# Optimization experiments

Hardware: AMD Instinct MI355X
Metric: run time of the kernel (lower is better)

## Reference

```python
import jax, jax.numpy as jnp
import numpy as np

MODEL_D = 512
N_HEADS = 8
D_K = 64
D_V = 64
EPS = 1e-5


def _layer_norm(x, g, b):
    mu = jnp.mean(x, axis=-1, keepdims=True)
    var = jnp.mean((x - mu) ** 2, axis=-1, keepdims=True)
    return (x - mu) * jax.lax.rsqrt(var + EPS) * g + b


def setup_inputs() -> dict:
    key = jax.random.key(0)
    ks = jax.random.split(key, 8)
    B, S = 8, 1024
    smiles = jax.random.normal(ks[0], (B, S, MODEL_D), dtype=jnp.float32)
    # causal mask: True where attention is disallowed (masked_fill semantics)
    mask = jnp.broadcast_to(jnp.triu(jnp.ones((S, S), dtype=bool), k=1), (B, S, S))
    sd = 1.0 / np.sqrt(MODEL_D)
    w_q = jax.random.normal(ks[1], (MODEL_D, N_HEADS * D_K), dtype=jnp.float32) * sd
    w_k = jax.random.normal(ks[2], (MODEL_D, N_HEADS * D_K), dtype=jnp.float32) * sd
    w_v = jax.random.normal(ks[3], (MODEL_D, N_HEADS * D_V), dtype=jnp.float32) * sd
    w_o = jax.random.normal(ks[4], (N_HEADS * D_V, MODEL_D), dtype=jnp.float32) * sd
    w1 = jax.random.normal(ks[5], (MODEL_D, 4 * MODEL_D), dtype=jnp.float32) * sd
    w2 = jax.random.normal(ks[6], (4 * MODEL_D, MODEL_D), dtype=jnp.float32) * (1.0 / np.sqrt(4 * MODEL_D))
    ln1_g = jnp.ones((MODEL_D,), jnp.float32)
    ln1_b = jnp.zeros((MODEL_D,), jnp.float32)
    ln2_g = jnp.ones((MODEL_D,), jnp.float32)
    ln2_b = jnp.zeros((MODEL_D,), jnp.float32)
    return {"smiles": smiles, "mask": mask, "w_q": w_q, "w_k": w_k, "w_v": w_v,
            "w_o": w_o, "ln1_g": ln1_g, "ln1_b": ln1_b, "w1": w1, "w2": w2,
            "ln2_g": ln2_g, "ln2_b": ln2_b}


def reference(smiles, mask, w_q, w_k, w_v, w_o, ln1_g, ln1_b, w1, w2, ln2_g, ln2_b):
    B, S, _ = smiles.shape
    # QKV projections -> [B, H, S, d]
    q = (smiles @ w_q).reshape(B, S, N_HEADS, D_K).transpose(0, 2, 1, 3)
    k = (smiles @ w_k).reshape(B, S, N_HEADS, D_K).transpose(0, 2, 1, 3)
    v = (smiles @ w_v).reshape(B, S, N_HEADS, D_V).transpose(0, 2, 1, 3)
    scores = jnp.einsum("bhqd,bhkd->bhqk", q, k) / np.sqrt(D_K)
    scores = jnp.where(mask[:, None, :, :], jnp.float32(-1e9), scores)
    attention = jax.nn.softmax(scores, axis=-1)
    ctx = jnp.einsum("bhqk,bhkd->bhqd", attention, v)
    ctx = ctx.transpose(0, 2, 1, 3).reshape(B, S, N_HEADS * D_V)
    attn_out = _layer_norm(ctx @ w_o + smiles, ln1_g, ln1_b)
    ffn = jax.nn.relu(attn_out @ w1) @ w2
    out = _layer_norm(ffn + attn_out, ln2_g, ln2_b)
    return out, attention
```

## Files before the change

kernel.cpp:

```cpp
#include <hip/hip_runtime.h>
#include <math.h>

#define BATCH 8
#define SEQ   1024
#define DMODEL 512
#define NHEADS 8
#define DKV   64
#define DFF   2048
#define ROWS  (BATCH * SEQ)
#define QKLD  1536

typedef __attribute__((ext_vector_type(8))) short short8;
typedef __attribute__((ext_vector_type(4))) float f32x4;

__device__ __forceinline__ short f2bf(float f) {
    unsigned u = __float_as_uint(f);
    u += 0x7FFFu + ((u >> 16) & 1u);
    return (short)(u >> 16);
}
__device__ __forceinline__ float bf2f(short s) {
    return __uint_as_float(((unsigned)(unsigned short)s) << 16);
}

#define GLD16(g, l) __builtin_amdgcn_global_load_lds( \
    (const __attribute__((address_space(1))) void*)(g), \
    (__attribute__((address_space(3))) void*)(l), 16, 0, 0)

__device__ __forceinline__ void stage128x32(const short* __restrict__ g, int ld,
                                            short* lds, int tid) {
    const int w = tid >> 6;
#pragma unroll
    for (int i = 0; i < 2; ++i) {
        const int L = i * 256 + tid;
        const int r = L >> 2, c = (L & 3) << 3;
        GLD16(g + (size_t)r * ld + c, lds + (size_t)(i * 256 + (w << 6)) * 8);
    }
}

template<int OUT_BF16, int RELU>
__global__ __launch_bounds__(256) void gemm_bt(const short* __restrict__ A,
                                               const short* __restrict__ Bt,
                                               void* __restrict__ Cv,
                                               int K, int lda, int ldb, int ldc,
                                               int qcols) {
    __shared__ short As[2][128 * 32];
    __shared__ short Bs[2][128 * 32];
    const int tid = threadIdx.x;

    const int nx = gridDim.x;
    const int nwg = nx * gridDim.y;
    const int flat = blockIdx.y * nx + blockIdx.x;
    const int swz = (flat & 7) * (nwg >> 3) + (flat >> 3);
    const int m0 = (swz / nx) * 128, n0 = (swz % nx) * 128;

    const int w = tid >> 6, lane = tid & 63;
    const int wr = (w >> 1) * 64, wc = (w & 1) * 64;
    const int lrow = lane & 15, hi = lane >> 4;

    f32x4 acc[4][4];
#pragma unroll
    for (int m = 0; m < 4; ++m)
#pragma unroll
        for (int n = 0; n < 4; ++n) acc[m][n] = {0.f, 0.f, 0.f, 0.f};

    const short* Ab = A + (size_t)m0 * lda;
    const short* Bb = Bt + (size_t)n0 * ldb;
    const int nt = K >> 5;

    stage128x32(Ab, lda, As[0], tid);
    stage128x32(Bb, ldb, Bs[0], tid);
    __syncthreads();

    int cur = 0;
    for (int t = 0; t < nt; ++t) {
        if (t + 1 < nt) {
            stage128x32(Ab + (size_t)(t + 1) * 32, lda, As[cur ^ 1], tid);
            stage128x32(Bb + (size_t)(t + 1) * 32, ldb, Bs[cur ^ 1], tid);
        }

        short8 af[4], bfr[4];
#pragma unroll
        for (int m = 0; m < 4; ++m)
            af[m] = *(const short8*)&As[cur][(size_t)(wr + m * 16 + lrow) * 32 + hi * 8];
#pragma unroll
        for (int n = 0; n < 4; ++n)
            bfr[n] = *(const short8*)&Bs[cur][(size_t)(wc + n * 16 + lrow) * 32 + hi * 8];
#pragma unroll
        for (int m = 0; m < 4; ++m)
#pragma unroll
            for (int n = 0; n < 4; ++n)
                acc[m][n] = __builtin_amdgcn_mfma_f32_16x16x32_bf16(bfr[n], af[m], acc[m][n], 0, 0, 0);

        __syncthreads();
        cur ^= 1;
    }

    const int orow = m0 + wr + lrow;
    const int ocol0 = n0 + wc + hi * 4;
#pragma unroll
    for (int m = 0; m < 4; ++m)
#pragma unroll
        for (int n = 0; n < 4; ++n) {
            const int col = ocol0 + n * 16;
            const float cs = (col < qcols) ? 0.125f : 1.0f;
            float v0 = acc[m][n][0], v1 = acc[m][n][1], v2 = acc[m][n][2], v3 = acc[m][n][3];
            if (RELU) {
                v0 = fmaxf(v0, 0.f); v1 = fmaxf(v1, 0.f);
                v2 = fmaxf(v2, 0.f); v3 = fmaxf(v3, 0.f);
            }
            v0 *= cs; v1 *= cs; v2 *= cs; v3 *= cs;
            const size_t off = (size_t)(orow + m * 16) * ldc + col;
            if (OUT_BF16) {
                short4 st = { f2bf(v0), f2bf(v1), f2bf(v2), f2bf(v3) };
                *(short4*)((short*)Cv + off) = st;
            } else {
                float4 st = { v0, v1, v2, v3 };
                *(float4*)((float*)Cv + off) = st;
            }
        }
}

__global__ __launch_bounds__(256, 2) void fused_attn(const short* __restrict__ Q,
                                                     const short* __restrict__ K,
                                                     const short* __restrict__ Vt,
                                                     float* __restrict__ attnP,
                                                     short* __restrict__ ctx) {
    const int flat = blockIdx.y * 8 + blockIdx.x;
    const int swz  = (flat & 7) * 64 + (flat >> 3);
    const int bh = swz >> 3, it = 7 - (swz & 7);
    const int b = bh >> 3, h = bh & 7;

    __shared__ short Qs[128 * 64];
    __shared__ short KVs[2][128 * 64];
    __shared__ short Ps[128 * 128];
    float* rsum = (float*)Ps;

    const int tid = threadIdx.x;
    const int w = tid >> 6, lane = tid & 63;
    const int wr = (w >> 1) * 64, wc2 = (w & 1);
    const int lrow = lane & 15, hi = lane >> 4;
    const size_t base = (size_t)b * SEQ * QKLD + h * DKV;
    float* aprow = attnP + (size_t)bh * SEQ * SEQ;

    auto stage_k = [&](int kt, short* dst) {
#pragma unroll
        for (int i = 0; i < 4; ++i) {
            const int L = i * 256 + tid;
            const int r = L >> 3, sc = ((L & 7) ^ (r & 7)) * 8;
            GLD16(K + base + (size_t)(kt * 128 + r) * QKLD + sc,
                  dst + (size_t)(i * 256 + (w << 6)) * 8);
        }
    };
    auto stage_v = [&](int kt, short* dst) {
#pragma unroll
        for (int i = 0; i < 4; ++i) {
            const int L = i * 256 + tid;
            const int r = L >> 4, sc = ((L & 15) ^ (r & 7)) * 8;
            GLD16(Vt + (size_t)(bh * DKV + r) * SEQ + kt * 128 + sc,
                  dst + (size_t)(i * 256 + (w << 6)) * 8);
        }
    };
    auto qkt = [&](const short* Ks, f32x4 s[4][4]) {
#pragma unroll
        for (int m = 0; m < 4; ++m)
#pragma unroll
            for (int n = 0; n < 4; ++n) s[m][n] = {0.f, 0.f, 0.f, 0.f};
#pragma unroll
        for (int sk = 0; sk < 2; ++sk) {
            short8 qf[4], kf[4];
#pragma unroll
            for (int m = 0; m < 4; ++m) {
                const int r = wr + m * 16 + lrow;
                qf[m] = *(const short8*)((const char*)Qs + r * 128 + ((hi * 16 + sk * 64) ^ ((r & 7) << 4)));
            }
#pragma unroll
            for (int n = 0; n < 4; ++n) {
                const int r = wc2 * 64 + n * 16 + lrow;
                kf[n] = *(const short8*)((const char*)Ks + r * 128 + ((hi * 16 + sk * 64) ^ ((r & 7) << 4)));
            }
#pragma unroll
            for (int m = 0; m < 4; ++m)
#pragma unroll
                for (int n = 0; n < 4; ++n)
                    s[m][n] = __builtin_amdgcn_mfma_f32_16x16x32_bf16(kf[n], qf[m], s[m][n], 0, 0, 0);
        }
    };

    {
        const int nz4 = (7 - it) * 32;
        if (nz4 > 0) {
            for (int r = tid >> 5; r < 128; r += 8) {
                float4* rp = (float4*)(aprow + (size_t)(it * 128 + r) * SEQ + (it + 1) * 128);
                for (int c = tid & 31; c < nz4; c += 32)
                    rp[c] = make_float4(0.f, 0.f, 0.f, 0.f);
            }
        }
    }

#pragma unroll
    for (int i = 0; i < 4; ++i) {
        const int L = i * 256 + tid;
        const int r = L >> 3, sc = ((L & 7) ^ (r & 7)) * 8;
        GLD16(Q + base + (size_t)(it * 128 + r) * QKLD + sc,
              Qs + (size_t)(i * 256 + (w << 6)) * 8);
    }
    stage_k(0, KVs[0]);
    stage_v(0, KVs[1]);
    __syncthreads();

    float rs[4] = {0.f, 0.f, 0.f, 0.f};
    f32x4 o[4][2];
#pragma unroll
    for (int m = 0; m < 4; ++m)
#pragma unroll
        for (int n = 0; n < 2; ++n) o[m][n] = {0.f, 0.f, 0.f, 0.f};

    for (int kt = 0; kt <= it; ++kt) {
        f32x4 s[4][4];
        qkt(KVs[0], s);

        const bool diag = (kt == it);
#pragma unroll
        for (int m = 0; m < 4; ++m) {
            const int q = wr + m * 16 + lrow;
#pragma unroll
            for (int n = 0; n < 4; ++n) {
                const int k0 = wc2 * 64 + n * 16 + hi * 4;
                float p0 = __expf(s[m][n][0]);
                float p1 = __expf(s[m][n][1]);
                float p2 = __expf(s[m][n][2]);
                float p3 = __expf(s[m][n][3]);
                if (diag) {
                    if (k0 + 0 > q) p0 = 0.f;
                    if (k0 + 1 > q) p1 = 0.f;
                    if (k0 + 2 > q) p2 = 0.f;
                    if (k0 + 3 > q) p3 = 0.f;
                }
                rs[m] += (p0 + p1) + (p2 + p3);
                short4 ph = { f2bf(p0), f2bf(p1), f2bf(p2), f2bf(p3) };
                *(short4*)((char*)Ps + q * 256 + ((k0 * 2) ^ ((q & 7) << 4))) = ph;
            }
        }
        __syncthreads();
        if (kt < it) stage_k(kt + 1, KVs[0]);

#pragma unroll
        for (int sk = 0; sk < 4; ++sk) {
            short8 pf[4], vf[2];
#pragma unroll
            for (int m = 0; m < 4; ++m) {
                const int r = wr + m * 16 + lrow;
                pf[m] = *(const short8*)((const char*)Ps + r * 256 + ((hi * 16 + sk * 64) ^ ((r & 7) << 4)));
            }
#pragma unroll
            for (int n = 0; n < 2; ++n) {
                const int r = wc2 * 32 + n * 16 + lrow;
                vf[n] = *(const short8*)((const char*)KVs[1] + r * 256 + ((hi * 16 + sk * 64) ^ ((r & 7) << 4)));
            }
#pragma unroll
            for (int m = 0; m < 4; ++m)
#pragma unroll
                for (int n = 0; n < 2; ++n)
                    o[m][n] = __builtin_amdgcn_mfma_f32_16x16x32_bf16(vf[n], pf[m], o[m][n], 0, 0, 0);
        }
        __syncthreads();
        if (kt < it) stage_v(kt + 1, KVs[1]);
    }

#pragma unroll
    for (int m = 0; m < 4; ++m) {
        rs[m] += __shfl_xor(rs[m], 16);
        rs[m] += __shfl_xor(rs[m], 32);
    }
    if (lane < 16) {
#pragma unroll
        for (int m = 0; m < 4; ++m)
            rsum[wc2 * 128 + wr + m * 16 + lane] = rs[m];
    }
    __syncthreads();
    if (tid < 128) rsum[tid] = 1.0f / (rsum[tid] + rsum[128 + tid]);
    __syncthreads();
    float inv[4];
#pragma unroll
    for (int m = 0; m < 4; ++m) inv[m] = rsum[wr + m * 16 + lrow];

#pragma unroll
    for (int m = 0; m < 4; ++m) {
        const int q = it * 128 + wr + m * 16 + lrow;
#pragma unroll
        for (int n = 0; n < 2; ++n) {
            const int d = h * DKV + wc2 * 32 + n * 16 + hi * 4;
            short4 st = { f2bf(o[m][n][0] * inv[m]), f2bf(o[m][n][1] * inv[m]),
                          f2bf(o[m][n][2] * inv[m]), f2bf(o[m][n][3] * inv[m]) };
            *(short4*)(ctx + (size_t)(b * SEQ + q) * DMODEL + d) = st;
        }
    }

    stage_k(0, KVs[0]);
    __syncthreads();
    int cur = 0;
    for (int kt = 0; kt <= it; ++kt) {
        if (kt < it) stage_k(kt + 1, KVs[cur ^ 1]);

        f32x4 s[4][4];
        qkt(KVs[cur], s);

        const bool diag = (kt == it);
#pragma unroll
        for (int m = 0; m < 4; ++m) {
            const int q = wr + m * 16 + lrow;
#pragma unroll
            for (int n = 0; n < 4; ++n) {
                const int k0 = wc2 * 64 + n * 16 + hi * 4;
                float p0 = __expf(s[m][n][0]);
                float p1 = __expf(s[m][n][1]);
                float p2 = __expf(s[m][n][2]);
                float p3 = __expf(s[m][n][3]);
                if (diag) {
                    if (k0 + 0 > q) p0 = 0.f;
                    if (k0 + 1 > q) p1 = 0.f;
                    if (k0 + 2 > q) p2 = 0.f;
                    if (k0 + 3 > q) p3 = 0.f;
                }
                float4 pv4 = { p0 * inv[m], p1 * inv[m], p2 * inv[m], p3 * inv[m] };
                *(float4*)(aprow + (size_t)(it * 128 + q) * SEQ + kt * 128 + k0) = pv4;
            }
        }
        __syncthreads();
        cur ^= 1;
    }
}

template<int RES_BF16, int OUT_F32, int OUT_BF16>
__global__ __launch_bounds__(128) void residual_ln(const float* __restrict__ xin,
                                                   const void* __restrict__ res,
                                                   const float* __restrict__ g,
                                                   const float* __restrict__ beta,
                                                   float* __restrict__ outf,
                                                   short* __restrict__ outh) {
    const int row = blockIdx.x;
    const int tid = threadIdx.x;

    float4 v = ((const float4*)(xin + (size_t)row * DMODEL))[tid];
    if (RES_BF16) {
        const short4 rr = ((const short4*)((const short*)res + (size_t)row * DMODEL))[tid];
        v.x += bf2f(rr.x); v.y += bf2f(rr.y); v.z += bf2f(rr.z); v.w += bf2f(rr.w);
    } else {
        const float4 rr = ((const float4*)((const float*)res + (size_t)row * DMODEL))[tid];
        v.x += rr.x; v.y += rr.y; v.z += rr.z; v.w += rr.w;
    }

    float sum = v.x + v.y + v.z + v.w;
    float sq  = v.x * v.x + v.y * v.y + v.z * v.z + v.w * v.w;
#pragma unroll
    for (int off = 32; off > 0; off >>= 1) {
        sum += __shfl_down(sum, off);
        sq  += __shfl_down(sq, off);
    }
    __shared__ float s_sum[2], s_sq[2];
    const int wid = tid >> 6, lane = tid & 63;
    if (lane == 0) { s_sum[wid] = sum; s_sq[wid] = sq; }
    __syncthreads();

    const float tsum = s_sum[0] + s_sum[1];
    const float tsq  = s_sq[0] + s_sq[1];
    const float mu   = tsum * (1.0f / DMODEL);
    const float var  = tsq * (1.0f / DMODEL) - mu * mu;
    const float rstd = rsqrtf(var + 1e-5f);

    const float4 gg = ((const float4*)g)[tid];
    const float4 bb = ((const float4*)beta)[tid];
    float4 o;
    o.x = (v.x - mu) * rstd * gg.x + bb.x;
    o.y = (v.y - mu) * rstd * gg.y + bb.y;
    o.z = (v.z - mu) * rstd * gg.z + bb.z;
    o.w = (v.w - mu) * rstd * gg.w + bb.w;
    if (OUT_F32) ((float4*)(outf + (size_t)row * DMODEL))[tid] = o;
    if (OUT_BF16) {
        short4 oh = { f2bf(o.x), f2bf(o.y), f2bf(o.z), f2bf(o.w) };
        ((short4*)(outh + (size_t)row * DMODEL))[tid] = oh;
    }
}

__global__ __launch_bounds__(256) void convert_bf16(const float* __restrict__ X,
                                                    short* __restrict__ Xh) {
    const size_t i = (size_t)blockIdx.x * 256 + threadIdx.x;
    const float4* p = (const float4*)X + i * 2;
    const float4 a = p[0], b = p[1];
    short8 o = { f2bf(a.x), f2bf(a.y), f2bf(a.z), f2bf(a.w),
                 f2bf(b.x), f2bf(b.y), f2bf(b.z), f2bf(b.w) };
    *(short8*)(Xh + i * 8) = o;
}

__global__ __launch_bounds__(256) void transpose_w(const float* __restrict__ W,
                                                   short* __restrict__ Wt,
                                                   int K, int N) {
    __shared__ float t[32][33];
    const int n0 = blockIdx.x * 32, k0 = blockIdx.y * 32;
    const int tx = threadIdx.x, ty = threadIdx.y;
#pragma unroll
    for (int i = 0; i < 4; ++i)
        t[ty + i * 8][tx] = W[(size_t)(k0 + ty + i * 8) * N + n0 + tx];
    __syncthreads();
#pragma unroll
    for (int i = 0; i < 4; ++i)
        Wt[(size_t)(n0 + ty + i * 8) * K + k0 + tx] = f2bf(t[tx][ty + i * 8]);
}

__global__ __launch_bounds__(256) void transpose_v(const short* __restrict__ QKV,
                                                   short* __restrict__ Vt) {
    __shared__ short t[32][33];
    const int s0 = blockIdx.x * 32, d0 = blockIdx.y * 32, bh = blockIdx.z;
    const int b = bh >> 3, h = bh & 7;
    const int tx = threadIdx.x, ty = threadIdx.y;
#pragma unroll
    for (int i = 0; i < 4; ++i)
        t[ty + i * 8][tx] = QKV[(size_t)(b * SEQ + s0 + ty + i * 8) * QKLD + 1024 + h * DKV + d0 + tx];
    __syncthreads();
#pragma unroll
    for (int i = 0; i < 4; ++i)
        Vt[(size_t)(bh * DKV + d0 + ty + i * 8) * SEQ + s0 + tx] = t[tx][ty + i * 8];
}

extern "C" void kernel_launch(void* const* d_in, const int* in_sizes, int n_in,
                              void* d_out, int out_size, void* d_ws, size_t ws_size,
                              hipStream_t stream) {
    const float* X    = (const float*)d_in[0];
    const float* w_q  = (const float*)d_in[2];
    const float* w_k  = (const float*)d_in[3];
    const float* w_v  = (const float*)d_in[4];
    const float* w_o  = (const float*)d_in[5];
    const float* ln1g = (const float*)d_in[6];
    const float* ln1b = (const float*)d_in[7];
    const float* w1   = (const float*)d_in[8];
    const float* w2   = (const float*)d_in[9];
    const float* ln2g = (const float*)d_in[10];
    const float* ln2b = (const float*)d_in[11];

    float* out   = (float*)d_out;
    float* attnP = out + (size_t)ROWS * DMODEL;

    const size_t M = 1u << 20;
    short* ws    = (short*)d_ws;
    short* qkv   = ws;
    short* Vt    = ws + 12 * M;
    short* ctxh  = ws + 16 * M;
    short* aoutH = ws + 20 * M;
    short* Xh    = ws + 24 * M;
    short* wqkvt = ws + 28 * M;
    short* wot   = wqkvt + 786432;
    short* w1t   = ws + 29 * M;
    short* w2t   = ws + 30 * M;
    short* hbuf  = ws;

    convert_bf16<<<dim3(2048), dim3(256), 0, stream>>>(X, Xh);
    transpose_w<<<dim3(16, 16), dim3(32, 8), 0, stream>>>(w_q, wqkvt, DMODEL, DMODEL);
    transpose_w<<<dim3(16, 16), dim3(32, 8), 0, stream>>>(w_k, wqkvt + 512 * 512, DMODEL, DMODEL);
    transpose_w<<<dim3(16, 16), dim3(32, 8), 0, stream>>>(w_v, wqkvt + 1024 * 512, DMODEL, DMODEL);
    transpose_w<<<dim3(16, 16), dim3(32, 8), 0, stream>>>(w_o, wot, DMODEL, DMODEL);
    transpose_w<<<dim3(64, 16), dim3(32, 8), 0, stream>>>(w1, w1t, DMODEL, DFF);
    transpose_w<<<dim3(16, 64), dim3(32, 8), 0, stream>>>(w2, w2t, DFF, DMODEL);

    gemm_bt<1, 0><<<dim3(12, 64), dim3(256), 0, stream>>>(Xh, wqkvt, qkv,
                                                          DMODEL, DMODEL, DMODEL, QKLD, 512);
    transpose_v<<<dim3(32, 2, 64), dim3(32, 8), 0, stream>>>(qkv, Vt);

    fused_attn<<<dim3(8, 64), dim3(256), 0, stream>>>(qkv, qkv + 512, Vt, attnP, ctxh);

    gemm_bt<0, 0><<<dim3(4, 64), dim3(256), 0, stream>>>(ctxh, wot, out,
                                                         DMODEL, DMODEL, DMODEL, DMODEL, 0);
    residual_ln<0, 0, 1><<<dim3(ROWS), dim3(128), 0, stream>>>(out, X, ln1g, ln1b, nullptr, aoutH);

    gemm_bt<1, 1><<<dim3(16, 64), dim3(256), 0, stream>>>(aoutH, w1t, hbuf,
                                                          DMODEL, DMODEL, DMODEL, DFF, 0);
    gemm_bt<0, 0><<<dim3(4, 64), dim3(256), 0, stream>>>(hbuf, w2t, out,
                                                         DFF, DFF, DFF, DMODEL, 0);
    residual_ln<1, 1, 0><<<dim3(ROWS), dim3(128), 0, stream>>>(out, aoutH, ln2g, ln2b, out, nullptr);
}
```

Before: 234.9 us.

## Fuse V transpose into QKV GEMM, merge prep kernels, use exp2 and nontemporal stores

The QKV GEMM epilogue now writes the V columns directly in transposed per-head layout, so the separate transpose_v kernel and the V section of the qkv buffer go away. The Q scale now folds in log2(e), which lets softmax use exp2f instead of __expf. The seven input conversion and weight transpose launches are merged into one prep_all kernel to cut launch overhead. Stores of the attention-probability matrix, both the values and the zero-filled masked region, become nontemporal to limit cache pollution. The strided 2-byte scattered stores in the V epilogue are poorly coalesced and could cost more than the transpose kernel they replace.

```diff
diff --git a/kernel.cpp b/kernel.cpp
--- a/kernel.cpp
+++ b/kernel.cpp
@@ -8,7 +8,8 @@
 #define DKV   64
 #define DFF   2048
 #define ROWS  (BATCH * SEQ)
-#define QKLD  1536
+#define QKLD  1024
+#define L2E_8 0.18033688011112042f
 
 typedef __attribute__((ext_vector_type(8))) short short8;
 typedef __attribute__((ext_vector_type(4))) float f32x4;
@@ -37,12 +38,12 @@
     }
 }
 
-template<int OUT_BF16, int RELU>
+template<int OUT_BF16, int RELU, int QKV_MODE>
 __global__ __launch_bounds__(256) void gemm_bt(const short* __restrict__ A,
                                                const short* __restrict__ Bt,
                                                void* __restrict__ Cv,
                                                int K, int lda, int ldb, int ldc,
-                                               int qcols) {
+                                               int qcols, short* __restrict__ Vt) {
     __shared__ short As[2][128 * 32];
     __shared__ short Bs[2][128 * 32];
     const int tid = threadIdx.x;
@@ -77,7 +78,6 @@
             stage128x32(Ab + (size_t)(t + 1) * 32, lda, As[cur ^ 1], tid);
             stage128x32(Bb + (size_t)(t + 1) * 32, ldb, Bs[cur ^ 1], tid);
         }
-
         short8 af[4], bfr[4];
 #pragma unroll
         for (int m = 0; m < 4; ++m)
@@ -90,19 +90,37 @@
 #pragma unroll
             for (int n = 0; n < 4; ++n)
                 acc[m][n] = __builtin_amdgcn_mfma_f32_16x16x32_bf16(bfr[n], af[m], acc[m][n], 0, 0, 0);
-
         __syncthreads();
         cur ^= 1;
     }
 
     const int orow = m0 + wr + lrow;
     const int ocol0 = n0 + wc + hi * 4;
+
+    if (QKV_MODE && n0 >= 1024) {
+#pragma unroll
+        for (int m = 0; m < 4; ++m) {
+            const int row = orow + m * 16;
+            const int b = row >> 10, s = row & 1023;
+#pragma unroll
+            for (int n = 0; n < 4; ++n) {
+                const int col = ocol0 + n * 16;
+                const int h = (col - 1024) >> 6, d = (col - 1024) & 63;
+                short* vp = Vt + ((size_t)((b << 3) + h) * 64 + d) * SEQ + s;
+#pragma unroll
+                for (int r = 0; r < 4; ++r)
+                    vp[(size_t)r * SEQ] = f2bf(acc[m][n][r]);
+            }
+        }
+        return;
+    }
+
 #pragma unroll
     for (int m = 0; m < 4; ++m)
 #pragma unroll
         for (int n = 0; n < 4; ++n) {
             const int col = ocol0 + n * 16;
-            const float cs = (col < qcols) ? 0.125f : 1.0f;
+            const float cs = (QKV_MODE && col < qcols) ? L2E_8 : 1.0f;
             float v0 = acc[m][n][0], v1 = acc[m][n][1], v2 = acc[m][n][2], v3 = acc[m][n][3];
             if (RELU) {
                 v0 = fmaxf(v0, 0.f); v1 = fmaxf(v1, 0.f);
@@ -189,10 +207,11 @@
     {
         const int nz4 = (7 - it) * 32;
         if (nz4 > 0) {
+            const f32x4 z = {0.f, 0.f, 0.f, 0.f};
             for (int r = tid >> 5; r < 128; r += 8) {
-                float4* rp = (float4*)(aprow + (size_t)(it * 128 + r) * SEQ + (it + 1) * 128);
+                f32x4* rp = (f32x4*)(aprow + (size_t)(it * 128 + r) * SEQ + (it + 1) * 128);
                 for (int c = tid & 31; c < nz4; c += 32)
-                    rp[c] = make_float4(0.f, 0.f, 0.f, 0.f);
+                    __builtin_nontemporal_store(z, rp + c);
             }
         }
     }
@@ -226,10 +245,10 @@
 #pragma unroll
             for (int n = 0; n < 4; ++n) {
                 const int k0 = wc2 * 64 + n * 16 + hi * 4;
-                float p0 = __expf(s[m][n][0]);
-                float p1 = __expf(s[m][n][1]);
-                float p2 = __expf(s[m][n][2]);
-                float p3 = __expf(s[m][n][3]);
+                float p0 = exp2f(s[m][n][0]);
+                float p1 = exp2f(s[m][n][1]);
+                float p2 = exp2f(s[m][n][2]);
+                float p3 = exp2f(s[m][n][3]);
                 if (diag) {
                     if (k0 + 0 > q) p0 = 0.f;
                     if (k0 + 1 > q) p1 = 0.f;
@@ -312,18 +331,19 @@
 #pragma unroll
             for (int n = 0; n < 4; ++n) {
                 const int k0 = wc2 * 64 + n * 16 + hi * 4;
-                float p0 = __expf(s[m][n][0]);
-                float p1 = __expf(s[m][n][1]);
-                float p2 = __expf(s[m][n][2]);
-                float p3 = __expf(s[m][n][3]);
+                float p0 = exp2f(s[m][n][0]);
+                float p1 = exp2f(s[m][n][1]);
+                float p2 = exp2f(s[m][n][2]);
+                float p3 = exp2f(s[m][n][3]);
                 if (diag) {
                     if (k0 + 0 > q) p0 = 0.f;
                     if (k0 + 1 > q) p1 = 0.f;
                     if (k0 + 2 > q) p2 = 0.f;
                     if (k0 + 3 > q) p3 = 0.f;
                 }
-                float4 pv4 = { p0 * inv[m], p1 * inv[m], p2 * inv[m], p3 * inv[m] };
-                *(float4*)(aprow + (size_t)(it * 128 + q) * SEQ + kt * 128 + k0) = pv4;
+                f32x4 pv4 = { p0 * inv[m], p1 * inv[m], p2 * inv[m], p3 * inv[m] };
+                __builtin_nontemporal_store(pv4,
+                    (f32x4*)(aprow + (size_t)(it * 128 + q) * SEQ + kt * 128 + k0));
             }
         }
         __syncthreads();
@@ -382,44 +402,51 @@
     }
 }
 
-__global__ __launch_bounds__(256) void convert_bf16(const float* __restrict__ X,
-                                                    short* __restrict__ Xh) {
-    const size_t i = (size_t)blockIdx.x * 256 + threadIdx.x;
-    const float4* p = (const float4*)X + i * 2;
-    const float4 a = p[0], b = p[1];
-    short8 o = { f2bf(a.x), f2bf(a.y), f2bf(a.z), f2bf(a.w),
-                 f2bf(b.x), f2bf(b.y), f2bf(b.z), f2bf(b.w) };
-    *(short8*)(Xh + i * 8) = o;
-}
-
-__global__ __launch_bounds__(256) void transpose_w(const float* __restrict__ W,
-                                                   short* __restrict__ Wt,
-                                                   int K, int N) {
-    __shared__ float t[32][33];
-    const int n0 = blockIdx.x * 32, k0 = blockIdx.y * 32;
-    const int tx = threadIdx.x, ty = threadIdx.y;
+__global__ __launch_bounds__(256) void prep_all(const float* __restrict__ X,
+                                                const float* __restrict__ w_q,
+                                                const float* __restrict__ w_k,
+                                                const float* __restrict__ w_v,
+                                                const float* __restrict__ w_o,
+                                                const float* __restrict__ w1,
+                                                const float* __restrict__ w2,
+                                                short* __restrict__ Xh,
+                                                short* __restrict__ wqkvt,
+                                                short* __restrict__ wot,
+                                                short* __restrict__ w1t,
+                                                short* __restrict__ w2t) {
+    const int flat = blockIdx.x;
+    const int tid = threadIdx.x;
+    if (flat < 2048) {
+        const size_t i = (size_t)flat * 256 + tid;
+        const float4* p = (const float4*)X + i * 2;
+        const float4 a = p[0], b = p[1];
+        short8 o = { f2bf(a.x), f2bf(a.y), f2bf(a.z), f2bf(a.w),
+                     f2bf(b.x), f2bf(b.y), f2bf(b.z), f2bf(b.w) };
+        *(short8*)(Xh + i * 8) = o;
+        return;
+    }
+    const int t = flat - 2048;
+    const float* W; short* Wt; int K, N, tile;
+    if (t < 1024) {
+        const int wsel = t >> 8; tile = t & 255;
+        K = 512; N = 512;
+        W  = (wsel == 0) ? w_q : (wsel == 1) ? w_k : (wsel == 2) ? w_v : w_o;
+        Wt = (wsel < 3) ? (wqkvt + (size_t)wsel * 512 * 512) : wot;
+    } else if (t < 2048) { tile = t - 1024; K = 512;  N = 2048; W = w1; Wt = w1t; }
+    else                 { tile = t - 2048; K = 2048; N = 512;  W = w2; Wt = w2t; }
+
+    const int ntx = N >> 5;
+    const int n0 = (tile % ntx) * 32, k0 = (tile / ntx) * 32;
+    const int tx = tid & 31, ty = tid >> 5;
+
+    __shared__ float tb[32][33];
 #pragma unroll
     for (int i = 0; i < 4; ++i)
-        t[ty + i * 8][tx] = W[(size_t)(k0 + ty + i * 8) * N + n0 + tx];
+        tb[ty + i * 8][tx] = W[(size_t)(k0 + ty + i * 8) * N + n0 + tx];
     __syncthreads();
 #pragma unroll
     for (int i = 0; i < 4; ++i)
-        Wt[(size_t)(n0 + ty + i * 8) * K + k0 + tx] = f2bf(t[tx][ty + i * 8]);
-}
-
-__global__ __launch_bounds__(256) void transpose_v(const short* __restrict__ QKV,
-                                                   short* __restrict__ Vt) {
-    __shared__ short t[32][33];
-    const int s0 = blockIdx.x * 32, d0 = blockIdx.y * 32, bh = blockIdx.z;
-    const int b = bh >> 3, h = bh & 7;
-    const int tx = threadIdx.x, ty = threadIdx.y;
-#pragma unroll
-    for (int i = 0; i < 4; ++i)
-        t[ty + i * 8][tx] = QKV[(size_t)(b * SEQ + s0 + ty + i * 8) * QKLD + 1024 + h * DKV + d0 + tx];
-    __syncthreads();
-#pragma unroll
-    for (int i = 0; i < 4; ++i)
-        Vt[(size_t)(bh * DKV + d0 + ty + i * 8) * SEQ + s0 + tx] = t[tx][ty + i * 8];
+        Wt[(size_t)(n0 + ty + i * 8) * K + k0 + tx] = f2bf(tb[tx][ty + i * 8]);
 }
 
 extern "C" void kernel_launch(void* const* d_in, const int* in_sizes, int n_in,
@@ -443,37 +470,31 @@
     const size_t M = 1u << 20;
     short* ws    = (short*)d_ws;
     short* qkv   = ws;
-    short* Vt    = ws + 12 * M;
-    short* ctxh  = ws + 16 * M;
-    short* aoutH = ws + 20 * M;
-    short* Xh    = ws + 24 * M;
-    short* wqkvt = ws + 28 * M;
+    short* Vt    = ws + 8 * M;
+    short* ctxh  = ws + 12 * M;
+    short* aoutH = ws + 16 * M;
+    short* Xh    = ws + 20 * M;
+    short* wqkvt = ws + 24 * M;
     short* wot   = wqkvt + 786432;
-    short* w1t   = ws + 29 * M;
-    short* w2t   = ws + 30 * M;
+    short* w1t   = ws + 25 * M;
+    short* w2t   = ws + 26 * M;
     short* hbuf  = ws;
 
-    convert_bf16<<<dim3(2048), dim3(256), 0, stream>>>(X, Xh);
-    transpose_w<<<dim3(16, 16), dim3(32, 8), 0, stream>>>(w_q, wqkvt, DMODEL, DMODEL);
-    transpose_w<<<dim3(16, 16), dim3(32, 8), 0, stream>>>(w_k, wqkvt + 512 * 512, DMODEL, DMODEL);
-    transpose_w<<<dim3(16, 16), dim3(32, 8), 0, stream>>>(w_v, wqkvt + 1024 * 512, DMODEL, DMODEL);
-    transpose_w<<<dim3(16, 16), dim3(32, 8), 0, stream>>>(w_o, wot, DMODEL, DMODEL);
-    transpose_w<<<dim3(64, 16), dim3(32, 8), 0, stream>>>(w1, w1t, DMODEL, DFF);
-    transpose_w<<<dim3(16, 64), dim3(32, 8), 0, stream>>>(w2, w2t, DFF, DMODEL);
-
-    gemm_bt<1, 0><<<dim3(12, 64), dim3(256), 0, stream>>>(Xh, wqkvt, qkv,
-                                                          DMODEL, DMODEL, DMODEL, QKLD, 512);
-    transpose_v<<<dim3(32, 2, 64), dim3(32, 8), 0, stream>>>(qkv, Vt);
+    prep_all<<<dim3(5120), dim3(256), 0, stream>>>(X, w_q, w_k, w_v, w_o, w1, w2,
+                                                   Xh, wqkvt, wot, w1t, w2t);
+
+    gemm_bt<1, 0, 1><<<dim3(12, 64), dim3(256), 0, stream>>>(Xh, wqkvt, qkv,
+                                                             DMODEL, DMODEL, DMODEL, QKLD, 512, Vt);
 
     fused_attn<<<dim3(8, 64), dim3(256), 0, stream>>>(qkv, qkv + 512, Vt, attnP, ctxh);
 
-    gemm_bt<0, 0><<<dim3(4, 64), dim3(256), 0, stream>>>(ctxh, wot, out,
-                                                         DMODEL, DMODEL, DMODEL, DMODEL, 0);
+    gemm_bt<0, 0, 0><<<dim3(4, 64), dim3(256), 0, stream>>>(ctxh, wot, out,
+                                                            DMODEL, DMODEL, DMODEL, DMODEL, 0, nullptr);
     residual_ln<0, 0, 1><<<dim3(ROWS), dim3(128), 0, stream>>>(out, X, ln1g, ln1b, nullptr, aoutH);
 
-    gemm_bt<1, 1><<<dim3(16, 64), dim3(256), 0, stream>>>(aoutH, w1t, hbuf,
-                                                          DMODEL, DMODEL, DMODEL, DFF, 0);
-    gemm_bt<0, 0><<<dim3(4, 64), dim3(256), 0, stream>>>(hbuf, w2t, out,
-                                                         DFF, DFF, DFF, DMODEL, 0);
+    gemm_bt<1, 1, 0><<<dim3(16, 64), dim3(256), 0, stream>>>(aoutH, w1t, hbuf,
+                                                             DMODEL, DMODEL, DMODEL, DFF, 0, nullptr);
+    gemm_bt<0, 0, 0><<<dim3(4, 64), dim3(256), 0, stream>>>(hbuf, w2t, out,
+                                                            DFF, DFF, DFF, DMODEL, 0, nullptr);
     residual_ln<1, 1, 0><<<dim3(ROWS), dim3(128), 0, stream>>>(out, aoutH, ln2g, ln2b, out, nullptr);
 }
```

Measured after the change: 230.2 us. -2.0%, faster.
